# Performance work log

Hardware: AMD Instinct MI355X
Metric: run time of the kernel (lower is better)

Reference implementation:

```python
import jax, jax.numpy as jnp
import numpy as np

N_C, N_F = 25000, 100000   # coarse / fine node counts
E_C, E_F = 100000, 400000  # coarse / fine edge counts
W, F_IN, F_OUT = 128, 128, 4


def _fnn2(x, w1, b1, w2, b2):
    # 2-layer FNN (fnns_depth=2) with SELU, dropout=0 (eval)
    return jax.nn.selu(x @ w1 + b1) @ w2 + b2


def _interaction(v, e, src, dst, n, ew1, eb1, ew2, eb2, nw1, nb1, nw2, nb2):
    # InteractionNetwork: edge update (gather) -> mean scatter -> node update, residuals
    e = _fnn2(jnp.concatenate([e, v[src], v[dst]], axis=-1), ew1, eb1, ew2, eb2) + e
    s = jax.ops.segment_sum(e, dst, num_segments=n)
    cnt = jax.ops.segment_sum(jnp.ones((e.shape[0], 1), e.dtype), dst, num_segments=n)
    agg = s / jnp.maximum(cnt, 1.0)  # 'mean' aggregation
    v = _fnn2(jnp.concatenate([v, agg], axis=-1), nw1, nb1, nw2, nb2) + v
    return v, e


def setup_inputs() -> dict:
    key = jax.random.key(0)
    ks = iter(jax.random.split(key, 64))
    def rn(shape, scale=1.0):
        return jax.random.normal(next(ks), shape, jnp.float32) * scale
    s3, s2, s1 = 1.0 / np.sqrt(3 * W), 1.0 / np.sqrt(2 * W), 1.0 / np.sqrt(W)
    d = {
        'v': rn((N_C, F_IN)),
        'c_coarse': rn((N_C, W)), 'c_fine': rn((N_F, W)),
        'e_coarse': rn((E_C, W)), 'e_fine': rn((E_F, W)),
        'rel_dist': rn((N_F, 1)),
        'ei_coarse': jax.random.randint(next(ks), (2, E_C), 0, N_C),
        'ei_fine': jax.random.randint(next(ks), (2, E_F), 0, N_F),
        'cluster': jax.random.randint(next(ks), (N_F,), 0, N_C),
        'in_node_w': rn((F_IN, W), 1.0 / np.sqrt(F_IN)), 'in_node_b': rn((W,), 0.01),
        'cond_w': rn((2, W, W), s1), 'cond_b': rn((2, W), 0.01),
        'edge_in_w': rn((2, W, W), s1), 'edge_in_b': rn((2, W), 0.01),
        'bn_ew1': rn((2, 3 * W, W), s3), 'bn_eb1': rn((2, W), 0.01),
        'bn_ew2': rn((2, W, W), s1), 'bn_eb2': rn((2, W), 0.01),
        'bn_nw1': rn((2, 2 * W, W), s2), 'bn_nb1': rn((2, W), 0.01),
        'bn_nw2': rn((2, W, W), s1), 'bn_nb2': rn((2, W), 0.01),
        'unp_w1': rn((W + 1, W), 1.0 / np.sqrt(W + 1)), 'unp_b1': rn((W,), 0.01),
        'unp_w2': rn((W, W), s1), 'unp_b2': rn((W,), 0.01),
        'up_ew1': rn((2, 3 * W, W), s3), 'up_eb1': rn((2, W), 0.01),
        'up_ew2': rn((2, W, W), s1), 'up_eb2': rn((2, W), 0.01),
        'up_nw1': rn((2, 2 * W, W), s2), 'up_nb1': rn((2, W), 0.01),
        'up_nw2': rn((2, W, W), s1), 'up_nb2': rn((2, W), 0.01),
        'out_w': rn((W, F_OUT), s1), 'out_b': rn((F_OUT,), 0.01),
    }
    return d


def reference(v, c_coarse, c_fine, e_coarse, e_fine, rel_dist, ei_coarse, ei_fine, cluster,
              in_node_w, in_node_b, cond_w, cond_b, edge_in_w, edge_in_b,
              bn_ew1, bn_eb1, bn_ew2, bn_eb2, bn_nw1, bn_nb1, bn_nw2, bn_nb2,
              unp_w1, unp_b1, unp_w2, unp_b2,
              up_ew1, up_eb1, up_ew2, up_eb2, up_nw1, up_nb1, up_nw2, up_nb2,
              out_w, out_b):
    src_c, dst_c = ei_coarse[0], ei_coarse[1]
    src_f, dst_f = ei_fine[0], ei_fine[1]
    # input projection + coarse-scale conditioning
    v = v @ in_node_w + in_node_b
    v = v + (c_coarse @ cond_w[0] + cond_b[0])
    e = e_coarse @ edge_in_w[0] + edge_in_b[0]
    # bottleneck InteractionNetwork blocks on coarse graph
    for i in range(bn_ew1.shape[0]):
        v, e = _interaction(v, e, src_c, dst_c, N_C,
                            bn_ew1[i], bn_eb1[i], bn_ew2[i], bn_eb2[i],
                            bn_nw1[i], bn_nb1[i], bn_nw2[i], bn_nb2[i])
    # up block: project skip conditioning/edges, unpool coarse->fine via cluster gather + FNN on [v, scalar rel pos]
    c = c_fine @ cond_w[1] + cond_b[1]
    e = e_fine @ edge_in_w[1] + edge_in_b[1]
    v = _fnn2(jnp.concatenate([v[cluster], rel_dist], axis=-1), unp_w1, unp_b1, unp_w2, unp_b2)
    v = v + c
    for i in range(up_ew1.shape[0]):
        v, e = _interaction(v, e, src_f, dst_f, N_F,
                            up_ew1[i], up_eb1[i], up_ew2[i], up_eb2[i],
                            up_nw1[i], up_nb1[i], up_nw2[i], up_nb2[i])
    return v @ out_w + out_b
```

## Files before the change

kernel.cpp:

```cpp
#include <hip/hip_runtime.h>
#include <hip/hip_bf16.h>

typedef __bf16 bf16_t;
typedef __bf16 bf16x8 __attribute__((ext_vector_type(8)));
typedef float f32x4 __attribute__((ext_vector_type(4)));

#define SELU_SCALE 1.0507009873554805f
#define SELU_ALPHA 1.6732632423543772f

__device__ __forceinline__ float selu_f(float x) {
    return x > 0.0f ? SELU_SCALE * x : SELU_SCALE * SELU_ALPHA * (__expf(x) - 1.0f);
}

__device__ __forceinline__ int4 load8(const void* p, size_t elem_off, int isf) {
    if (!isf) return *(const int4*)((const bf16_t*)p + elem_off);
    const float* f = (const float*)p + elem_off;
    float4 a = ((const float4*)f)[0], b = ((const float4*)f)[1];
    union { int4 i; bf16_t h[8]; } u;
    u.h[0] = (bf16_t)a.x; u.h[1] = (bf16_t)a.y; u.h[2] = (bf16_t)a.z; u.h[3] = (bf16_t)a.w;
    u.h[4] = (bf16_t)b.x; u.h[5] = (bf16_t)b.y; u.h[6] = (bf16_t)b.z; u.h[7] = (bf16_t)b.w;
    return u.i;
}

__global__ void detect_dtype(const unsigned short* p, int* flag) {
    if (threadIdx.x == 0) {
        float m = 0.0f;
        for (int i = 0; i < 128; i++) {
            unsigned int u = ((unsigned int)p[i]) << 16;
            float v = __uint_as_float(u);
            v = fabsf(v);
            if (!(v <= 1e3f)) { m = 1e30f; break; }
            m = fmaxf(m, v);
        }
        *flag = (m > 1e3f) ? 1 : 0;
    }
}

struct VDesc { const void* s; bf16_t* d; int eoff; int n; };
struct VArgs { VDesc v[19]; };
__global__ void convert_vecs(VArgs a, const int* __restrict__ flag) {
    int isf = *flag;
    VDesc vd = a.v[blockIdx.y];
    int i = blockIdx.x * 256 + threadIdx.x;
    if (i < vd.n) {
        size_t idx = (size_t)vd.eoff + i;
        vd.d[i] = isf ? (bf16_t)(((const float*)vd.s)[idx]) : ((const bf16_t*)vd.s)[idx];
    }
}

struct TDesc { const void* s; bf16_t* d; int eoff; int Ksrc; int Ktot; int koff; };
struct TArgs { TDesc t[23]; };
__global__ void transpose_all(TArgs a, const int* __restrict__ flag) {
    int isf = *flag;
    TDesc td = a.t[blockIdx.y];
    int i = blockIdx.x * 256 + threadIdx.x;
    if (i < 128 * td.Ksrc) {
        int n = i / td.Ksrc;
        int k = i - n * td.Ksrc;
        size_t si = (size_t)td.eoff + (size_t)k * 128 + n;
        bf16_t v = isf ? (bf16_t)(((const float*)td.s)[si]) : ((const bf16_t*)td.s)[si];
        td.d[(size_t)n * td.Ktot + td.koff + k] = v;
    }
}

__global__ void count_dst(const int* __restrict__ dst, int* __restrict__ cnt, int E) {
    int e = blockIdx.x * 256 + threadIdx.x;
    if (e < E) atomicAdd(&cnt[dst[e]], 1);
}

__global__ void seg_alloc(const int* __restrict__ cnt, int* __restrict__ rp,
                          int* __restrict__ total, int n) {
    int i = blockIdx.x * 256 + threadIdx.x;
    if (i < n) rp[i] = atomicAdd(total, cnt[i]);
}

__global__ void init_cursor(const int* __restrict__ rp, int* __restrict__ cur, int n) {
    int i = blockIdx.x * 256 + threadIdx.x;
    if (i < n) cur[i] = rp[i];
}

__global__ void csr_scatter(const int* __restrict__ dst, int* __restrict__ cur,
                            int* __restrict__ eids, int E) {
    int e = blockIdx.x * 256 + threadIdx.x;
    if (e < E) {
        unsigned s = (unsigned)atomicAdd(&cur[dst[e]], 1);
        if (s < (unsigned)E) eids[s] = e;
    }
}

template<int K>
__global__ __launch_bounds__(256) void lin1(
    int M, const void* __restrict__ A0, const void* __restrict__ A1,
    const bf16_t* __restrict__ Wt, const bf16_t* __restrict__ b1,
    const bf16_t* __restrict__ b2, const bf16_t* __restrict__ res,
    bf16_t* __restrict__ out, const int* __restrict__ flag)
{
    constexpr int SA = K + 8;
    __shared__ bf16_t sA[64 * SA];
    const int isf = *flag;
    const int tid = threadIdx.x;
    const int row0 = blockIdx.x * 64;
    const int lane16 = tid & 15;
    const int rgrp = tid >> 4;

    #pragma unroll
    for (int chunk = 0; chunk < K; chunk += 128) {
        const void* sp = chunk ? A1 : A0;
        for (int r = rgrp; r < 64; r += 16) {
            int rr = row0 + r; if (rr >= M) rr = M - 1;
            int4 u = load8(sp, (size_t)rr * 128 + lane16 * 8, isf);
            *(int4*)&sA[r * SA + chunk + lane16 * 8] = u;
        }
    }
    __syncthreads();

    const int lane = tid & 63, wave = tid >> 6;
    const int l15 = lane & 15, lk = lane >> 4;
    const int colbase = wave * 32;
    f32x4 acc[4][2];
    const f32x4 zero = {0.f, 0.f, 0.f, 0.f};
    for (int rt = 0; rt < 4; rt++) { acc[rt][0] = zero; acc[rt][1] = zero; }

    #pragma unroll
    for (int k0 = 0; k0 < K; k0 += 32) {
        bf16x8 w0 = *(const bf16x8*)(Wt + (size_t)(colbase + l15) * K + k0 + lk * 8);
        bf16x8 w1 = *(const bf16x8*)(Wt + (size_t)(colbase + 16 + l15) * K + k0 + lk * 8);
        #pragma unroll
        for (int rt = 0; rt < 4; rt++) {
            bf16x8 av = *(const bf16x8*)(&sA[(rt * 16 + l15) * SA + k0 + lk * 8]);
            acc[rt][0] = __builtin_amdgcn_mfma_f32_16x16x32_bf16(av, w0, acc[rt][0], 0, 0, 0);
            acc[rt][1] = __builtin_amdgcn_mfma_f32_16x16x32_bf16(av, w1, acc[rt][1], 0, 0, 0);
        }
    }

    #pragma unroll
    for (int rt = 0; rt < 4; rt++)
        #pragma unroll
        for (int ct = 0; ct < 2; ct++) {
            int col = colbase + ct * 16 + l15;
            float bc = (float)b1[col] + (b2 ? (float)b2[col] : 0.0f);
            #pragma unroll
            for (int r = 0; r < 4; r++) {
                int grow = row0 + rt * 16 + lk * 4 + r;
                if (grow < M) {
                    float x = acc[rt][ct][r] + bc;
                    if (res) x += (float)res[(size_t)grow * 128 + col];
                    out[(size_t)grow * 128 + col] = (bf16_t)x;
                }
            }
        }
}

template<int K>
__global__ __launch_bounds__(512, (K == 384) ? 6 : 8) void fnn2k(
    int mode, int M,
    const bf16_t* __restrict__ A0, const bf16_t* __restrict__ V,
    const int* __restrict__ g0, const int* __restrict__ g1,
    const bf16_t* __restrict__ Emat, const int* __restrict__ rp,
    const int* __restrict__ degc, const int* __restrict__ eids,
    const bf16_t* __restrict__ W1t, const bf16_t* __restrict__ b1,
    const bf16_t* __restrict__ W2t, const bf16_t* __restrict__ b2,
    const bf16_t* __restrict__ relb, const bf16_t* __restrict__ w1last,
    const bf16_t* __restrict__ res, bf16_t* __restrict__ out,
    const bf16_t* __restrict__ finw, const bf16_t* __restrict__ finb,
    void* __restrict__ fout, const int* __restrict__ flag)
{
    constexpr int CH = K / 128;
    constexpr int PL = 64 * 136;
    __shared__ bf16_t sA[CH * PL];
    bf16_t* sH = sA + (CH - 1) * PL;

    const int isf = *flag;
    const int tid = threadIdx.x;
    const int lane16 = tid & 15;
    const int rgrp = tid >> 4;
    const int lane = tid & 63, wave = tid >> 6;
    const int l15 = lane & 15, lk = lane >> 4;
    const int colbase = wave * 16;
    const int row0 = blockIdx.x * 64;
    const bool res_lds = (res == A0) && (CH > 1);
    const f32x4 zero = {0.f, 0.f, 0.f, 0.f};

    #pragma unroll
    for (int c = 0; c < CH; c++) {
        if (mode == 2 && c == 1) {
            #pragma unroll
            for (int i = 0; i < 2; i++) {
                int r = rgrp + i * 32;
                int rr = row0 + r; if (rr >= M) rr = M - 1;
                int beg = rp[rr], deg = degc[rr];
                float a8[8] = {0.f, 0.f, 0.f, 0.f, 0.f, 0.f, 0.f, 0.f};
                for (int e = 0; e < deg; e++) {
                    int eid = eids[beg + e];
                    bf16x8 ev = *(const bf16x8*)(Emat + (size_t)eid * 128 + lane16 * 8);
                    #pragma unroll
                    for (int j = 0; j < 8; j++) a8[j] += (float)ev[j];
                }
                float inv = 1.0f / (float)(deg > 0 ? deg : 1);
                union { int4 i4; bf16_t h[8]; } w;
                #pragma unroll
                for (int j = 0; j < 8; j++) w.h[j] = (bf16_t)(a8[j] * inv);
                *(int4*)&sA[c * PL + r * 136 + lane16 * 8] = w.i4;
            }
        } else {
            #pragma unroll
            for (int i = 0; i < 2; i++) {
                int r = rgrp + i * 32;
                int rr = row0 + r; if (rr >= M) rr = M - 1;
                const bf16_t* sp;
                if (mode == 1)
                    sp = (c == 0) ? A0 + (size_t)rr * 128
                       : (c == 1) ? V + (size_t)g0[rr] * 128
                                  : V + (size_t)g1[rr] * 128;
                else if (mode == 3) sp = A0 + (size_t)g0[rr] * 128;
                else sp = A0 + (size_t)rr * 128;
                *(int4*)&sA[c * PL + r * 136 + lane16 * 8] = *(const int4*)(sp + lane16 * 8);
            }
        }
    }
    __syncthreads();

    f32x4 acc[4];
    #pragma unroll
    for (int rt = 0; rt < 4; rt++) acc[rt] = zero;
    #pragma unroll
    for (int k0 = 0; k0 < K; k0 += 32) {
        bf16x8 w0 = *(const bf16x8*)(W1t + (size_t)(colbase + l15) * K + k0 + lk * 8);
        #pragma unroll
        for (int rt = 0; rt < 4; rt++) {
            bf16x8 av = *(const bf16x8*)(&sA[(k0 / 128) * PL + (rt * 16 + l15) * 136 + (k0 & 127) + lk * 8]);
            acc[rt] = __builtin_amdgcn_mfma_f32_16x16x32_bf16(av, w0, acc[rt], 0, 0, 0);
        }
    }
    __syncthreads();

    {
        int col = colbase + l15;
        float b1c = (float)b1[col];
        float wlc = (mode == 3) ? (float)w1last[col] : 0.0f;
        #pragma unroll
        for (int rt = 0; rt < 4; rt++)
            #pragma unroll
            for (int r = 0; r < 4; r++) {
                int lrow = rt * 16 + lk * 4 + r;
                int grow = row0 + lrow;
                float x = acc[rt][r] + b1c;
                if (mode == 3) {
                    float rv = (grow < M) ? (float)relb[grow] : 0.0f;
                    x += rv * wlc;
                }
                x = selu_f(x);
                sH[lrow * 136 + col] = (bf16_t)x;
            }
    }
    __syncthreads();

    f32x4 acc2[4];
    #pragma unroll
    for (int rt = 0; rt < 4; rt++) acc2[rt] = zero;
    #pragma unroll
    for (int k0 = 0; k0 < 128; k0 += 32) {
        bf16x8 w0 = *(const bf16x8*)(W2t + (size_t)(colbase + l15) * 128 + k0 + lk * 8);
        #pragma unroll
        for (int rt = 0; rt < 4; rt++) {
            bf16x8 av = *(const bf16x8*)(&sH[(rt * 16 + l15) * 136 + k0 + lk * 8]);
            acc2[rt] = __builtin_amdgcn_mfma_f32_16x16x32_bf16(av, w0, acc2[rt], 0, 0, 0);
        }
    }
    if (finw) __syncthreads();

    {
        int col = colbase + l15;
        float b2c = (float)b2[col];
        #pragma unroll
        for (int rt = 0; rt < 4; rt++)
            #pragma unroll
            for (int r = 0; r < 4; r++) {
                int lrow = rt * 16 + lk * 4 + r;
                int grow = row0 + lrow;
                if (grow < M) {
                    float x = acc2[rt][r] + b2c;
                    if (res) {
                        float rv = res_lds ? (float)sA[lrow * 136 + col]
                                           : (float)res[(size_t)grow * 128 + col];
                        x += rv;
                    }
                    bf16_t xb = (bf16_t)x;
                    if (out) out[(size_t)grow * 128 + col] = xb;
                    if (finw) sH[lrow * 136 + col] = xb;
                }
            }
    }

    if (finw) {
        __syncthreads();
        if (tid < 256) {
            int orow = tid >> 2, c = tid & 3;
            int grow = row0 + orow;
            if (grow < M) {
                float s = (float)finb[c];
                #pragma unroll
                for (int k = 0; k < 128; k++)
                    s += (float)sH[orow * 136 + k] * (float)finw[k * 4 + c];
                if (isf) ((float*)fout)[(size_t)grow * 4 + c] = s;
                else     ((bf16_t*)fout)[(size_t)grow * 4 + c] = (bf16_t)s;
            }
        }
    }
}

extern "C" void kernel_launch(void* const* d_in, const int* in_sizes, int n_in,
                              void* d_out, int out_size, void* d_ws, size_t ws_size,
                              hipStream_t stream) {
    const int NC = 25000, NF = 100000, EC = 100000, EF = 400000;

    const void* v_in      = d_in[0];
    const void* c_coarse  = d_in[1];
    const void* c_fine    = d_in[2];
    const void* e_coarse  = d_in[3];
    const void* e_fine    = d_in[4];
    const void* rel_dist  = d_in[5];
    const int*  ei_c      = (const int*)d_in[6];
    const int*  ei_f      = (const int*)d_in[7];
    const int*  cluster   = (const int*)d_in[8];
    const void* in_node_w = d_in[9];
    const void* in_node_b = d_in[10];
    const void* cond_w    = d_in[11];
    const void* cond_b    = d_in[12];
    const void* edge_in_w = d_in[13];
    const void* edge_in_b = d_in[14];
    const void* bn_ew1    = d_in[15];
    const void* bn_eb1    = d_in[16];
    const void* bn_ew2    = d_in[17];
    const void* bn_eb2    = d_in[18];
    const void* bn_nw1    = d_in[19];
    const void* bn_nb1    = d_in[20];
    const void* bn_nw2    = d_in[21];
    const void* bn_nb2    = d_in[22];
    const void* unp_w1    = d_in[23];
    const void* unp_b1    = d_in[24];
    const void* unp_w2    = d_in[25];
    const void* unp_b2    = d_in[26];
    const void* up_ew1    = d_in[27];
    const void* up_eb1    = d_in[28];
    const void* up_ew2    = d_in[29];
    const void* up_eb2    = d_in[30];
    const void* up_nw1    = d_in[31];
    const void* up_nb1    = d_in[32];
    const void* up_nw2    = d_in[33];
    const void* up_nb2    = d_in[34];
    const void* out_w     = d_in[35];
    const void* out_b     = d_in[36];

    const int* src_c = ei_c, * dst_c = ei_c + EC;
    const int* src_f = ei_f, * dst_f = ei_f + EF;

    char* base = (char*)d_ws;
    size_t off = 0;
    auto carve = [&](size_t bytes) -> void* {
        void* p = base + off;
        off += (bytes + 255) & ~(size_t)255;
        return p;
    };
    int*    flag   = (int*)carve(256);
    int*    totals = (int*)carve(256);
    bf16_t* vc     = (bf16_t*)carve((size_t)NC * 128 * 2);
    bf16_t* vf     = (bf16_t*)carve((size_t)NF * 128 * 2);
    bf16_t* ef     = (bf16_t*)carve((size_t)EF * 128 * 2);
    bf16_t* ec     = ef;
    int*    cnti_c = (int*)carve((size_t)NC * 4);
    int*    cnti_f = (int*)carve((size_t)NF * 4);
    int*    rp_c   = (int*)carve((size_t)NC * 4);
    int*    rp_f   = (int*)carve((size_t)NF * 4);
    int*    cur_c  = (int*)carve((size_t)NC * 4);
    int*    cur_f  = (int*)carve((size_t)NF * 4);

    auto cw = [&](size_t elems) -> bf16_t* { return (bf16_t*)carve(elems * 2); };
    bf16_t* Wic    = cw(128 * 256);
    bf16_t* Wein0  = cw(128 * 128);
    bf16_t* Wein1  = cw(128 * 128);
    bf16_t* Wcond1 = cw(128 * 128);
    bf16_t* Wbe1[2] = { cw(128 * 384), cw(128 * 384) };
    bf16_t* Wbe2[2] = { cw(128 * 128), cw(128 * 128) };
    bf16_t* Wbn1[2] = { cw(128 * 256), cw(128 * 256) };
    bf16_t* Wbn2[2] = { cw(128 * 128), cw(128 * 128) };
    bf16_t* Wunp1 = cw(128 * 128);
    bf16_t* Wunp2 = cw(128 * 128);
    bf16_t* Wue1[2] = { cw(128 * 384), cw(128 * 384) };
    bf16_t* Wue2[2] = { cw(128 * 128), cw(128 * 128) };
    bf16_t* Wun1[2] = { cw(128 * 256), cw(128 * 256) };
    bf16_t* Wun2[2] = { cw(128 * 128), cw(128 * 128) };
    bf16_t* b_in   = cw(128);
    bf16_t* b_cond = cw(256);
    bf16_t* b_ein  = cw(256);
    bf16_t* b_be1  = cw(256);
    bf16_t* b_be2  = cw(256);
    bf16_t* b_bn1  = cw(256);
    bf16_t* b_bn2  = cw(256);
    bf16_t* b_unp1 = cw(128);
    bf16_t* b_unp2 = cw(128);
    bf16_t* b_ue1  = cw(256);
    bf16_t* b_ue2  = cw(256);
    bf16_t* b_un1  = cw(256);
    bf16_t* b_un2  = cw(256);
    bf16_t* b_out  = cw(8);
    bf16_t* w1last = cw(128);
    bf16_t* relb   = cw(NF);
    bf16_t* foutw  = cw(512);
    int*    eids_c = (int*)carve((size_t)EC * 4);
    int*    eids_f = (int*)carve((size_t)EF * 4);

    detect_dtype<<<1, 64, 0, stream>>>((const unsigned short*)in_node_b, flag);

    VArgs va; int vi = 0;
    auto addV = [&](const void* s, bf16_t* d, int eoff, int n) {
        va.v[vi].s = s; va.v[vi].d = d; va.v[vi].eoff = eoff; va.v[vi].n = n; vi++;
    };
    addV(in_node_b, b_in, 0, 128);
    addV(cond_b, b_cond, 0, 256);
    addV(edge_in_b, b_ein, 0, 256);
    addV(bn_eb1, b_be1, 0, 256);  addV(bn_eb2, b_be2, 0, 256);
    addV(bn_nb1, b_bn1, 0, 256);  addV(bn_nb2, b_bn2, 0, 256);
    addV(unp_b1, b_unp1, 0, 128); addV(unp_b2, b_unp2, 0, 128);
    addV(up_eb1, b_ue1, 0, 256);  addV(up_eb2, b_ue2, 0, 256);
    addV(up_nb1, b_un1, 0, 256);  addV(up_nb2, b_un2, 0, 256);
    addV(out_b, b_out, 0, 4);
    addV(unp_w1, w1last, 128 * 128, 128);
    addV(rel_dist, relb, 0, NF);
    addV(out_w, foutw, 0, 512);
    dim3 vg((NF + 255) / 256, vi);
    convert_vecs<<<vg, 256, 0, stream>>>(va, flag);

    TArgs ta; int ti = 0;
    auto addT = [&](const void* s, bf16_t* d, int eoff, int Ksrc, int Ktot, int koff) {
        ta.t[ti].s = s; ta.t[ti].d = d; ta.t[ti].eoff = eoff;
        ta.t[ti].Ksrc = Ksrc; ta.t[ti].Ktot = Ktot; ta.t[ti].koff = koff; ti++;
    };
    addT(in_node_w, Wic, 0, 128, 256, 0);
    addT(cond_w,    Wic, 0, 128, 256, 128);
    addT(edge_in_w, Wein0, 0, 128, 128, 0);
    addT(edge_in_w, Wein1, 16384, 128, 128, 0);
    addT(cond_w,    Wcond1, 16384, 128, 128, 0);
    for (int i = 0; i < 2; i++) {
        addT(bn_ew1, Wbe1[i], i * 49152, 384, 384, 0);
        addT(bn_ew2, Wbe2[i], i * 16384, 128, 128, 0);
        addT(bn_nw1, Wbn1[i], i * 32768, 256, 256, 0);
        addT(bn_nw2, Wbn2[i], i * 16384, 128, 128, 0);
        addT(up_ew1, Wue1[i], i * 49152, 384, 384, 0);
        addT(up_ew2, Wue2[i], i * 16384, 128, 128, 0);
        addT(up_nw1, Wun1[i], i * 32768, 256, 256, 0);
        addT(up_nw2, Wun2[i], i * 16384, 128, 128, 0);
    }
    addT(unp_w1, Wunp1, 0, 128, 128, 0);
    addT(unp_w2, Wunp2, 0, 128, 128, 0);
    dim3 tg((128 * 384 + 255) / 256, ti);
    transpose_all<<<tg, 256, 0, stream>>>(ta, flag);

    hipMemsetAsync(cnti_c, 0, (size_t)NC * 4, stream);
    hipMemsetAsync(cnti_f, 0, (size_t)NF * 4, stream);
    hipMemsetAsync(totals, 0, 256, stream);
    count_dst<<<(EC + 255) / 256, 256, 0, stream>>>(dst_c, cnti_c, EC);
    count_dst<<<(EF + 255) / 256, 256, 0, stream>>>(dst_f, cnti_f, EF);
    seg_alloc<<<(NC + 255) / 256, 256, 0, stream>>>(cnti_c, rp_c, totals + 0, NC);
    seg_alloc<<<(NF + 255) / 256, 256, 0, stream>>>(cnti_f, rp_f, totals + 1, NF);
    init_cursor<<<(NC + 255) / 256, 256, 0, stream>>>(rp_c, cur_c, NC);
    init_cursor<<<(NF + 255) / 256, 256, 0, stream>>>(rp_f, cur_f, NF);
    csr_scatter<<<(EC + 255) / 256, 256, 0, stream>>>(dst_c, cur_c, eids_c, EC);
    csr_scatter<<<(EF + 255) / 256, 256, 0, stream>>>(dst_f, cur_f, eids_f, EF);

    lin1<256><<<(NC + 63) / 64, 256, 0, stream>>>(NC, v_in, c_coarse, Wic, b_in, b_cond,
                                                  nullptr, vc, flag);
    lin1<128><<<(EC + 63) / 64, 256, 0, stream>>>(EC, e_coarse, nullptr, Wein0, b_ein,
                                                  nullptr, nullptr, ec, flag);

    for (int i = 0; i < 2; i++) {
        fnn2k<384><<<(EC + 63) / 64, 512, 0, stream>>>(
            1, EC, ec, vc, src_c, dst_c, nullptr, nullptr, nullptr, nullptr,
            Wbe1[i], b_be1 + i * 128, Wbe2[i], b_be2 + i * 128,
            nullptr, nullptr, ec, ec,
            nullptr, nullptr, nullptr, flag);
        fnn2k<256><<<(NC + 63) / 64, 512, 0, stream>>>(
            2, NC, vc, nullptr, nullptr, nullptr, ec, rp_c, cnti_c, eids_c,
            Wbn1[i], b_bn1 + i * 128, Wbn2[i], b_bn2 + i * 128,
            nullptr, nullptr, vc, vc,
            nullptr, nullptr, nullptr, flag);
    }

    lin1<128><<<(NF + 63) / 64, 256, 0, stream>>>(NF, c_fine, nullptr, Wcond1, b_cond + 128,
                                                  nullptr, nullptr, vf, flag);
    fnn2k<128><<<(NF + 63) / 64, 512, 0, stream>>>(
        3, NF, vc, nullptr, cluster, nullptr, nullptr, nullptr, nullptr, nullptr,
        Wunp1, b_unp1, Wunp2, b_unp2,
        relb, w1last, vf, vf,
        nullptr, nullptr, nullptr, flag);
    lin1<128><<<(EF + 63) / 64, 256, 0, stream>>>(EF, e_fine, nullptr, Wein1, b_ein + 128,
                                                  nullptr, nullptr, ef, flag);

    for (int i = 0; i < 2; i++) {
        fnn2k<384><<<(EF + 63) / 64, 512, 0, stream>>>(
            1, EF, ef, vf, src_f, dst_f, nullptr, nullptr, nullptr, nullptr,
            Wue1[i], b_ue1 + i * 128, Wue2[i], b_ue2 + i * 128,
            nullptr, nullptr, ef, ef,
            nullptr, nullptr, nullptr, flag);
        int last = (i == 1);
        fnn2k<256><<<(NF + 63) / 64, 512, 0, stream>>>(
            2, NF, vf, nullptr, nullptr, nullptr, ef, rp_f, cnti_f, eids_f,
            Wun1[i], b_un1 + i * 128, Wun2[i], b_un2 + i * 128,
            nullptr, nullptr, vf, (last ? nullptr : vf),
            (last ? foutw : nullptr), b_out,
            (last ? d_out : nullptr), flag);
    }
}
```

Measured before the change: 878.9 us.

## Precompute per-node src/dst projections to shrink edge MLP first-layer GEMM

The edge MLP's first layer over [e, v[src], v[dst]] is split algebraically: v@W_src and v@W_dst are computed once per node into a 256-wide buffer, then each edge gathers and sums the two projected rows and adds them to a K=128 GEMM on e. This moves edge-count GEMM work (K=384) down to K=128 plus a node-count GEMM, and cuts LDS use so occupancy can rise. It adds an extra kernel and an intermediate buffer per block, and rounds the projections to bf16 before summing, which changes numerics slightly.

```diff
diff --git a/kernel.cpp b/kernel.cpp
--- a/kernel.cpp
+++ b/kernel.cpp
@@ -49,7 +49,7 @@
 }
 
 struct TDesc { const void* s; bf16_t* d; int eoff; int Ksrc; int Ktot; int koff; };
-struct TArgs { TDesc t[23]; };
+struct TArgs { TDesc t[31]; };
 __global__ void transpose_all(TArgs a, const int* __restrict__ flag) {
     int isf = *flag;
     TDesc td = a.t[blockIdx.y];
@@ -88,7 +88,7 @@
     }
 }
 
-template<int K>
+template<int K, int N>
 __global__ __launch_bounds__(256) void lin1(
     int M, const void* __restrict__ A0, const void* __restrict__ A1,
     const bf16_t* __restrict__ Wt, const bf16_t* __restrict__ b1,
@@ -96,6 +96,7 @@
     bf16_t* __restrict__ out, const int* __restrict__ flag)
 {
     constexpr int SA = K + 8;
+    constexpr int NCT = N / 64;
     __shared__ bf16_t sA[64 * SA];
     const int isf = *flag;
     const int tid = threadIdx.x;
@@ -116,27 +117,31 @@
 
     const int lane = tid & 63, wave = tid >> 6;
     const int l15 = lane & 15, lk = lane >> 4;
-    const int colbase = wave * 32;
-    f32x4 acc[4][2];
+    const int colbase = wave * (N / 4);
+    f32x4 acc[4][NCT];
     const f32x4 zero = {0.f, 0.f, 0.f, 0.f};
-    for (int rt = 0; rt < 4; rt++) { acc[rt][0] = zero; acc[rt][1] = zero; }
+    for (int rt = 0; rt < 4; rt++)
+        for (int ct = 0; ct < NCT; ct++) acc[rt][ct] = zero;
 
     #pragma unroll
     for (int k0 = 0; k0 < K; k0 += 32) {
-        bf16x8 w0 = *(const bf16x8*)(Wt + (size_t)(colbase + l15) * K + k0 + lk * 8);
-        bf16x8 w1 = *(const bf16x8*)(Wt + (size_t)(colbase + 16 + l15) * K + k0 + lk * 8);
+        bf16x8 wv[NCT];
+        #pragma unroll
+        for (int ct = 0; ct < NCT; ct++)
+            wv[ct] = *(const bf16x8*)(Wt + (size_t)(colbase + ct * 16 + l15) * K + k0 + lk * 8);
         #pragma unroll
         for (int rt = 0; rt < 4; rt++) {
             bf16x8 av = *(const bf16x8*)(&sA[(rt * 16 + l15) * SA + k0 + lk * 8]);
-            acc[rt][0] = __builtin_amdgcn_mfma_f32_16x16x32_bf16(av, w0, acc[rt][0], 0, 0, 0);
-            acc[rt][1] = __builtin_amdgcn_mfma_f32_16x16x32_bf16(av, w1, acc[rt][1], 0, 0, 0);
+            #pragma unroll
+            for (int ct = 0; ct < NCT; ct++)
+                acc[rt][ct] = __builtin_amdgcn_mfma_f32_16x16x32_bf16(av, wv[ct], acc[rt][ct], 0, 0, 0);
         }
     }
 
     #pragma unroll
     for (int rt = 0; rt < 4; rt++)
         #pragma unroll
-        for (int ct = 0; ct < 2; ct++) {
+        for (int ct = 0; ct < NCT; ct++) {
             int col = colbase + ct * 16 + l15;
             float bc = (float)b1[col] + (b2 ? (float)b2[col] : 0.0f);
             #pragma unroll
@@ -144,17 +149,17 @@
                 int grow = row0 + rt * 16 + lk * 4 + r;
                 if (grow < M) {
                     float x = acc[rt][ct][r] + bc;
-                    if (res) x += (float)res[(size_t)grow * 128 + col];
-                    out[(size_t)grow * 128 + col] = (bf16_t)x;
+                    if (res) x += (float)res[(size_t)grow * N + col];
+                    out[(size_t)grow * N + col] = (bf16_t)x;
                 }
             }
         }
 }
 
-template<int K>
-__global__ __launch_bounds__(512, (K == 384) ? 6 : 8) void fnn2k(
-    int mode, int M,
-    const bf16_t* __restrict__ A0, const bf16_t* __restrict__ V,
+template<int MODE>
+__global__ __launch_bounds__(512, 8) void fnn2k(
+    int M,
+    const bf16_t* __restrict__ A0, const bf16_t* __restrict__ Psd,
     const int* __restrict__ g0, const int* __restrict__ g1,
     const bf16_t* __restrict__ Emat, const int* __restrict__ rp,
     const int* __restrict__ degc, const int* __restrict__ eids,
@@ -165,10 +170,11 @@
     const bf16_t* __restrict__ finw, const bf16_t* __restrict__ finb,
     void* __restrict__ fout, const int* __restrict__ flag)
 {
-    constexpr int CH = K / 128;
+    constexpr int NP = (MODE == 3) ? 1 : 2;
+    constexpr int K1 = (MODE == 2) ? 256 : 128;
     constexpr int PL = 64 * 136;
-    __shared__ bf16_t sA[CH * PL];
-    bf16_t* sH = sA + (CH - 1) * PL;
+    __shared__ bf16_t sA[NP * PL];
+    bf16_t* sH = sA + (NP - 1) * PL;
 
     const int isf = *flag;
     const int tid = threadIdx.x;
@@ -178,16 +184,24 @@
     const int l15 = lane & 15, lk = lane >> 4;
     const int colbase = wave * 16;
     const int row0 = blockIdx.x * 64;
-    const bool res_lds = (res == A0) && (CH > 1);
+    const bool res_lds = (res == A0);
     const f32x4 zero = {0.f, 0.f, 0.f, 0.f};
 
     #pragma unroll
-    for (int c = 0; c < CH; c++) {
-        if (mode == 2 && c == 1) {
-            #pragma unroll
-            for (int i = 0; i < 2; i++) {
-                int r = rgrp + i * 32;
-                int rr = row0 + r; if (rr >= M) rr = M - 1;
+    for (int c = 0; c < NP; c++) {
+        #pragma unroll
+        for (int i = 0; i < 2; i++) {
+            int r = rgrp + i * 32;
+            int rr = row0 + r; if (rr >= M) rr = M - 1;
+            int4 u;
+            if (MODE == 1 && c == 1) {
+                bf16x8 pa = *(const bf16x8*)(Psd + (size_t)g0[rr] * 256 + lane16 * 8);
+                bf16x8 pb = *(const bf16x8*)(Psd + (size_t)g1[rr] * 256 + 128 + lane16 * 8);
+                union { int4 i4; bf16_t h[8]; } w;
+                #pragma unroll
+                for (int j = 0; j < 8; j++) w.h[j] = (bf16_t)((float)pa[j] + (float)pb[j]);
+                u = w.i4;
+            } else if (MODE == 2 && c == 1) {
                 int beg = rp[rr], deg = degc[rr];
                 float a8[8] = {0.f, 0.f, 0.f, 0.f, 0.f, 0.f, 0.f, 0.f};
                 for (int e = 0; e < deg; e++) {
@@ -200,22 +214,13 @@
                 union { int4 i4; bf16_t h[8]; } w;
                 #pragma unroll
                 for (int j = 0; j < 8; j++) w.h[j] = (bf16_t)(a8[j] * inv);
-                *(int4*)&sA[c * PL + r * 136 + lane16 * 8] = w.i4;
+                u = w.i4;
+            } else {
+                const bf16_t* sp = (MODE == 3) ? A0 + (size_t)g0[rr] * 128
+                                               : A0 + (size_t)rr * 128;
+                u = *(const int4*)(sp + lane16 * 8);
             }
-        } else {
-            #pragma unroll
-            for (int i = 0; i < 2; i++) {
-                int r = rgrp + i * 32;
-                int rr = row0 + r; if (rr >= M) rr = M - 1;
-                const bf16_t* sp;
-                if (mode == 1)
-                    sp = (c == 0) ? A0 + (size_t)rr * 128
-                       : (c == 1) ? V + (size_t)g0[rr] * 128
-                                  : V + (size_t)g1[rr] * 128;
-                else if (mode == 3) sp = A0 + (size_t)g0[rr] * 128;
-                else sp = A0 + (size_t)rr * 128;
-                *(int4*)&sA[c * PL + r * 136 + lane16 * 8] = *(const int4*)(sp + lane16 * 8);
-            }
+            *(int4*)&sA[c * PL + r * 136 + lane16 * 8] = u;
         }
     }
     __syncthreads();
@@ -224,20 +229,20 @@
     #pragma unroll
     for (int rt = 0; rt < 4; rt++) acc[rt] = zero;
     #pragma unroll
-    for (int k0 = 0; k0 < K; k0 += 32) {
-        bf16x8 w0 = *(const bf16x8*)(W1t + (size_t)(colbase + l15) * K + k0 + lk * 8);
+    for (int k0 = 0; k0 < K1; k0 += 32) {
+        bf16x8 w0 = *(const bf16x8*)(W1t + (size_t)(colbase + l15) * K1 + k0 + lk * 8);
         #pragma unroll
         for (int rt = 0; rt < 4; rt++) {
             bf16x8 av = *(const bf16x8*)(&sA[(k0 / 128) * PL + (rt * 16 + l15) * 136 + (k0 & 127) + lk * 8]);
             acc[rt] = __builtin_amdgcn_mfma_f32_16x16x32_bf16(av, w0, acc[rt], 0, 0, 0);
         }
     }
-    __syncthreads();
+    if (MODE != 1) __syncthreads();
 
     {
         int col = colbase + l15;
         float b1c = (float)b1[col];
-        float wlc = (mode == 3) ? (float)w1last[col] : 0.0f;
+        float wlc = (MODE == 3) ? (float)w1last[col] : 0.0f;
         #pragma unroll
         for (int rt = 0; rt < 4; rt++)
             #pragma unroll
@@ -245,7 +250,8 @@
                 int lrow = rt * 16 + lk * 4 + r;
                 int grow = row0 + lrow;
                 float x = acc[rt][r] + b1c;
-                if (mode == 3) {
+                if (MODE == 1) x += (float)sH[lrow * 136 + col];
+                if (MODE == 3) {
                     float rv = (grow < M) ? (float)relb[grow] : 0.0f;
                     x += rv * wlc;
                 }
@@ -281,8 +287,8 @@
                 if (grow < M) {
                     float x = acc2[rt][r] + b2c;
                     if (res) {
-                        float rv = res_lds ? (float)sA[lrow * 136 + col]
-                                           : (float)res[(size_t)grow * 128 + col];
+                        float rv = (res_lds && NP > 1) ? (float)sA[lrow * 136 + col]
+                                                       : (float)res[(size_t)grow * 128 + col];
                         x += rv;
                     }
                     bf16_t xb = (bf16_t)x;
@@ -363,11 +369,13 @@
         return p;
     };
     int*    flag   = (int*)carve(256);
+    int*    zflag  = (int*)carve(256);
     int*    totals = (int*)carve(256);
     bf16_t* vc     = (bf16_t*)carve((size_t)NC * 128 * 2);
     bf16_t* vf     = (bf16_t*)carve((size_t)NF * 128 * 2);
     bf16_t* ef     = (bf16_t*)carve((size_t)EF * 128 * 2);
     bf16_t* ec     = ef;
+    bf16_t* Psd    = (bf16_t*)carve((size_t)NF * 256 * 2);
     int*    cnti_c = (int*)carve((size_t)NC * 4);
     int*    cnti_f = (int*)carve((size_t)NF * 4);
     int*    rp_c   = (int*)carve((size_t)NC * 4);
@@ -380,13 +388,15 @@
     bf16_t* Wein0  = cw(128 * 128);
     bf16_t* Wein1  = cw(128 * 128);
     bf16_t* Wcond1 = cw(128 * 128);
-    bf16_t* Wbe1[2] = { cw(128 * 384), cw(128 * 384) };
+    bf16_t* Wbe1[2] = { cw(128 * 128), cw(128 * 128) };
+    bf16_t* Wsd_c[2] = { cw(256 * 128), cw(256 * 128) };
     bf16_t* Wbe2[2] = { cw(128 * 128), cw(128 * 128) };
     bf16_t* Wbn1[2] = { cw(128 * 256), cw(128 * 256) };
     bf16_t* Wbn2[2] = { cw(128 * 128), cw(128 * 128) };
     bf16_t* Wunp1 = cw(128 * 128);
     bf16_t* Wunp2 = cw(128 * 128);
-    bf16_t* Wue1[2] = { cw(128 * 384), cw(128 * 384) };
+    bf16_t* Wue1[2] = { cw(128 * 128), cw(128 * 128) };
+    bf16_t* Wsd_f[2] = { cw(256 * 128), cw(256 * 128) };
     bf16_t* Wue2[2] = { cw(128 * 128), cw(128 * 128) };
     bf16_t* Wun1[2] = { cw(128 * 256), cw(128 * 256) };
     bf16_t* Wun2[2] = { cw(128 * 128), cw(128 * 128) };
@@ -407,10 +417,13 @@
     bf16_t* w1last = cw(128);
     bf16_t* relb   = cw(NF);
     bf16_t* foutw  = cw(512);
+    bf16_t* zerob  = cw(256);
     int*    eids_c = (int*)carve((size_t)EC * 4);
     int*    eids_f = (int*)carve((size_t)EF * 4);
 
     detect_dtype<<<1, 64, 0, stream>>>((const unsigned short*)in_node_b, flag);
+    hipMemsetAsync(zflag, 0, 256, stream);
+    hipMemsetAsync(zerob, 0, 512, stream);
 
     VArgs va; int vi = 0;
     auto addV = [&](const void* s, bf16_t* d, int eoff, int n) {
@@ -442,18 +455,22 @@
     addT(edge_in_w, Wein1, 16384, 128, 128, 0);
     addT(cond_w,    Wcond1, 16384, 128, 128, 0);
     for (int i = 0; i < 2; i++) {
-        addT(bn_ew1, Wbe1[i], i * 49152, 384, 384, 0);
+        addT(bn_ew1, Wbe1[i],           i * 49152,         128, 128, 0);
+        addT(bn_ew1, Wsd_c[i],          i * 49152 + 16384, 128, 128, 0);
+        addT(bn_ew1, Wsd_c[i] + 16384,  i * 49152 + 32768, 128, 128, 0);
         addT(bn_ew2, Wbe2[i], i * 16384, 128, 128, 0);
         addT(bn_nw1, Wbn1[i], i * 32768, 256, 256, 0);
         addT(bn_nw2, Wbn2[i], i * 16384, 128, 128, 0);
-        addT(up_ew1, Wue1[i], i * 49152, 384, 384, 0);
+        addT(up_ew1, Wue1[i],           i * 49152,         128, 128, 0);
+        addT(up_ew1, Wsd_f[i],          i * 49152 + 16384, 128, 128, 0);
+        addT(up_ew1, Wsd_f[i] + 16384,  i * 49152 + 32768, 128, 128, 0);
         addT(up_ew2, Wue2[i], i * 16384, 128, 128, 0);
         addT(up_nw1, Wun1[i], i * 32768, 256, 256, 0);
         addT(up_nw2, Wun2[i], i * 16384, 128, 128, 0);
     }
     addT(unp_w1, Wunp1, 0, 128, 128, 0);
     addT(unp_w2, Wunp2, 0, 128, 128, 0);
-    dim3 tg((128 * 384 + 255) / 256, ti);
+    dim3 tg((128 * 256 + 255) / 256, ti);
     transpose_all<<<tg, 256, 0, stream>>>(ta, flag);
 
     hipMemsetAsync(cnti_c, 0, (size_t)NC * 4, stream);
@@ -468,43 +485,43 @@
     csr_scatter<<<(EC + 255) / 256, 256, 0, stream>>>(dst_c, cur_c, eids_c, EC);
     csr_scatter<<<(EF + 255) / 256, 256, 0, stream>>>(dst_f, cur_f, eids_f, EF);
 
-    lin1<256><<<(NC + 63) / 64, 256, 0, stream>>>(NC, v_in, c_coarse, Wic, b_in, b_cond,
-                                                  nullptr, vc, flag);
-    lin1<128><<<(EC + 63) / 64, 256, 0, stream>>>(EC, e_coarse, nullptr, Wein0, b_ein,
-                                                  nullptr, nullptr, ec, flag);
+    lin1<256, 128><<<(NC + 63) / 64, 256, 0, stream>>>(NC, v_in, c_coarse, Wic, b_in, b_cond,
+                                                       nullptr, vc, flag);
+    lin1<128, 128><<<(EC + 63) / 64, 256, 0, stream>>>(EC, e_coarse, nullptr, Wein0, b_ein,
+                                                       nullptr, nullptr, ec, flag);
 
     for (int i = 0; i < 2; i++) {
-        fnn2k<384><<<(EC + 63) / 64, 512, 0, stream>>>(
-            1, EC, ec, vc, src_c, dst_c, nullptr, nullptr, nullptr, nullptr,
+        lin1<128, 256><<<(NC + 63) / 64, 256, 0, stream>>>(NC, vc, nullptr, Wsd_c[i], zerob,
+                                                           nullptr, nullptr, Psd, zflag);
+        fnn2k<1><<<(EC + 63) / 64, 512, 0, stream>>>(
+            EC, ec, Psd, src_c, dst_c, nullptr, nullptr, nullptr, nullptr,
             Wbe1[i], b_be1 + i * 128, Wbe2[i], b_be2 + i * 128,
-            nullptr, nullptr, ec, ec,
-            nullptr, nullptr, nullptr, flag);
-        fnn2k<256><<<(NC + 63) / 64, 512, 0, stream>>>(
-            2, NC, vc, nullptr, nullptr, nullptr, ec, rp_c, cnti_c, eids_c,
+            nullptr, nullptr, ec, ec, nullptr, nullptr, nullptr, flag);
+        fnn2k<2><<<(NC + 63) / 64, 512, 0, stream>>>(
+            NC, vc, nullptr, nullptr, nullptr, ec, rp_c, cnti_c, eids_c,
             Wbn1[i], b_bn1 + i * 128, Wbn2[i], b_bn2 + i * 128,
-            nullptr, nullptr, vc, vc,
-            nullptr, nullptr, nullptr, flag);
-    }
-
-    lin1<128><<<(NF + 63) / 64, 256, 0, stream>>>(NF, c_fine, nullptr, Wcond1, b_cond + 128,
-                                                  nullptr, nullptr, vf, flag);
-    fnn2k<128><<<(NF + 63) / 64, 512, 0, stream>>>(
-        3, NF, vc, nullptr, cluster, nullptr, nullptr, nullptr, nullptr, nullptr,
+            nullptr, nullptr, vc, vc, nullptr, nullptr, nullptr, flag);
+    }
+
+    lin1<128, 128><<<(NF + 63) / 64, 256, 0, stream>>>(NF, c_fine, nullptr, Wcond1, b_cond + 128,
+                                                       nullptr, nullptr, vf, flag);
+    fnn2k<3><<<(NF + 63) / 64, 512, 0, stream>>>(
+        NF, vc, nullptr, cluster, nullptr, nullptr, nullptr, nullptr, nullptr,
         Wunp1, b_unp1, Wunp2, b_unp2,
-        relb, w1last, vf, vf,
-        nullptr, nullptr, nullptr, flag);
-    lin1<128><<<(EF + 63) / 64, 256, 0, stream>>>(EF, e_fine, nullptr, Wein1, b_ein + 128,
-                                                  nullptr, nullptr, ef, flag);
+        relb, w1last, vf, vf, nullptr, nullptr, nullptr, flag);
+    lin1<128, 128><<<(EF + 63) / 64, 256, 0, stream>>>(EF, e_fine, nullptr, Wein1, b_ein + 128,
+                                                       nullptr, nullptr, ef, flag);
 
     for (int i = 0; i < 2; i++) {
-        fnn2k<384><<<(EF + 63) / 64, 512, 0, stream>>>(
-            1, EF, ef, vf, src_f, dst_f, nullptr, nullptr, nullptr, nullptr,
+        lin1<128, 256><<<(NF + 63) / 64, 256, 0, stream>>>(NF, vf, nullptr, Wsd_f[i], zerob,
+                                                           nullptr, nullptr, Psd, zflag);
+        fnn2k<1><<<(EF + 63) / 64, 512, 0, stream>>>(
+            EF, ef, Psd, src_f, dst_f, nullptr, nullptr, nullptr, nullptr,
             Wue1[i], b_ue1 + i * 128, Wue2[i], b_ue2 + i * 128,
-            nullptr, nullptr, ef, ef,
-            nullptr, nullptr, nullptr, flag);
+            nullptr, nullptr, ef, ef, nullptr, nullptr, nullptr, flag);
         int last = (i == 1);
-        fnn2k<256><<<(NF + 63) / 64, 512, 0, stream>>>(
-            2, NF, vf, nullptr, nullptr, nullptr, ef, rp_f, cnti_f, eids_f,
+        fnn2k<2><<<(NF + 63) / 64, 512, 0, stream>>>(
+            NF, vf, nullptr, nullptr, nullptr, ef, rp_f, cnti_f, eids_f,
             Wun1[i], b_un1 + i * 128, Wun2[i], b_un2 + i * 128,
             nullptr, nullptr, vf, (last ? nullptr : vf),
             (last ? foutw : nullptr), b_out,
```

Result: faster. 809.3 us (-7.9%).
